# Kernel optimization log

Hardware: AMD Instinct MI355X
Metric: run time of the kernel (lower is better)

Reference implementation:

```python
import jax, jax.numpy as jnp
import numpy as np


def _maxpool(x, k):
    # non-overlapping kxk max pool (kernel == stride), NCHW
    B, C, H, W = x.shape
    return x.reshape(B, C, H // k, k, W // k, k).max(axis=(3, 5))


def setup_inputs() -> dict:
    key = jax.random.key(0)
    k1, k2, k3, k4 = jax.random.split(key, 4)
    return {
        "x1": jax.random.normal(k1, (8, 128, 128, 128), dtype=jnp.float32),
        "x2": jax.random.normal(k2, (8, 32, 256, 256), dtype=jnp.float32),
        "x3": jax.random.normal(k3, (8, 2, 512, 512), dtype=jnp.float32),
        "pure_ff": jax.random.normal(k4, (8, 256, 64, 64), dtype=jnp.float32),
    }


def reference(x1, x2, x3, pure_ff):
    # torch.cat([x,x],1) repeated n times duplicates the whole channel block
    # 2^n times; pooling duplicated channels equals pooling once then tiling.
    y1 = jnp.tile(_maxpool(x1, 2), (1, 2, 1, 1))    # 1 cat  -> x2 channels
    y2 = jnp.tile(_maxpool(x2, 4), (1, 8, 1, 1))    # 3 cats -> x8 channels
    y3 = jnp.tile(_maxpool(x3, 8), (1, 128, 1, 1))  # 7 cats -> x128 channels
    return jax.nn.relu(y1 + y2 + y3 + pure_ff)
```

## Files before the change

kernel.cpp:

```cpp
#include <hip/hip_runtime.h>
#include <math.h>


__global__ __launch_bounds__(256, 8) void fused_ff_block3(
    const float* __restrict__ x1, const float* __restrict__ x2,
    const float* __restrict__ x3, const float* __restrict__ ff,
    float* __restrict__ out)
{
    __shared__ float y2s[32][16];
    __shared__ float y3s[2][16];

    const int bid = blockIdx.x;
    const int wq  = bid & 3;
    const int h   = (bid >> 2) & 63;
    const int b   = bid >> 8;
    const int tid = threadIdx.x;

    const int lane = tid & 63;
    const int o3   = (tid >> 6) * 8 + (lane >> 3);
    const int r3   = lane & 7;
    const int c3   = o3 >> 4;
    const int w3   = o3 & 15;
    const float* p3 = x3 + (size_t)b * 524288 + (size_t)c3 * 262144
                    + (size_t)(h * 8 + r3) * 512 + (size_t)(wq * 16 + w3) * 8;
    const float4 a3 = *reinterpret_cast<const float4*>(p3);
    const float4 b3 = *reinterpret_cast<const float4*>(p3 + 4);

    #pragma unroll
    for (int it = 0; it < 2; ++it) {
        const int v  = tid + it * 256;
        const int c2 = v >> 4;
        const int w2 = v & 15;
        const float* p = x2 + (size_t)b * 2097152 + (size_t)c2 * 65536
                       + (size_t)(h * 4) * 256 + (size_t)(wq * 16 + w2) * 4;
        const float4 q0 = *reinterpret_cast<const float4*>(p);
        const float4 q1 = *reinterpret_cast<const float4*>(p + 256);
        const float4 q2 = *reinterpret_cast<const float4*>(p + 512);
        const float4 q3 = *reinterpret_cast<const float4*>(p + 768);
        float m = fmaxf(fmaxf(fmaxf(q0.x, q0.y), fmaxf(q0.z, q0.w)),
                        fmaxf(fmaxf(q1.x, q1.y), fmaxf(q1.z, q1.w)));
        m = fmaxf(m, fmaxf(fmaxf(q2.x, q2.y), fmaxf(q2.z, q2.w)));
        m = fmaxf(m, fmaxf(fmaxf(q3.x, q3.y), fmaxf(q3.z, q3.w)));
        y2s[c2][w2] = m;
    }

    float m3 = fmaxf(fmaxf(fmaxf(a3.x, a3.y), fmaxf(a3.z, a3.w)),
                     fmaxf(fmaxf(b3.x, b3.y), fmaxf(b3.z, b3.w)));
    m3 = fmaxf(m3, __shfl_xor(m3, 1, 64));
    m3 = fmaxf(m3, __shfl_xor(m3, 2, 64));
    m3 = fmaxf(m3, __shfl_xor(m3, 4, 64));
    if (r3 == 0) y3s[c3][w3] = m3;

    __syncthreads();

    const int w4  = tid & 3;
    const int c1b = tid >> 2;
    #pragma unroll
    for (int it = 0; it < 2; ++it) {
        const int c1 = c1b + it * 64;
        const float* p = x1 + (size_t)b * 2097152 + (size_t)c1 * 16384
                       + (size_t)(h * 2) * 128 + (size_t)(wq * 16 + w4 * 4) * 2;
        const float4 a0 = *reinterpret_cast<const float4*>(p);
        const float4 a1 = *reinterpret_cast<const float4*>(p + 4);
        const float4 r0 = *reinterpret_cast<const float4*>(p + 128);
        const float4 r1 = *reinterpret_cast<const float4*>(p + 132);
        float4 y1v;
        y1v.x = fmaxf(fmaxf(a0.x, a0.y), fmaxf(r0.x, r0.y));
        y1v.y = fmaxf(fmaxf(a0.z, a0.w), fmaxf(r0.z, r0.w));
        y1v.z = fmaxf(fmaxf(a1.x, a1.y), fmaxf(r1.x, r1.y));
        y1v.w = fmaxf(fmaxf(a1.z, a1.w), fmaxf(r1.z, r1.w));

        const float4 y2v = *reinterpret_cast<const float4*>(&y2s[c1 & 31][w4 * 4]);
        const float4 y3v = *reinterpret_cast<const float4*>(&y3s[c1 & 1][w4 * 4]);

        const size_t o0 = (size_t)b * 1048576 + (size_t)c1 * 4096
                        + (size_t)h * 64 + (size_t)(wq * 16 + w4 * 4);
        const size_t o1 = o0 + (size_t)128 * 4096;
        const float4 f0 = *reinterpret_cast<const float4*>(ff + o0);
        const float4 f1 = *reinterpret_cast<const float4*>(ff + o1);

        float4 s;
        s.x = y1v.x + y2v.x + y3v.x;
        s.y = y1v.y + y2v.y + y3v.y;
        s.z = y1v.z + y2v.z + y3v.z;
        s.w = y1v.w + y2v.w + y3v.w;

        float4 u0, u1;
        u0.x = fmaxf(s.x + f0.x, 0.0f);
        u0.y = fmaxf(s.y + f0.y, 0.0f);
        u0.z = fmaxf(s.z + f0.z, 0.0f);
        u0.w = fmaxf(s.w + f0.w, 0.0f);
        u1.x = fmaxf(s.x + f1.x, 0.0f);
        u1.y = fmaxf(s.y + f1.y, 0.0f);
        u1.z = fmaxf(s.z + f1.z, 0.0f);
        u1.w = fmaxf(s.w + f1.w, 0.0f);

        *reinterpret_cast<float4*>(out + o0) = u0;
        *reinterpret_cast<float4*>(out + o1) = u1;
    }
}

extern "C" void kernel_launch(void* const* d_in, const int* in_sizes, int n_in,
                              void* d_out, int out_size, void* d_ws, size_t ws_size,
                              hipStream_t stream) {
    const float* x1 = (const float*)d_in[0];
    const float* x2 = (const float*)d_in[1];
    const float* x3 = (const float*)d_in[2];
    const float* ff = (const float*)d_in[3];
    float* out = (float*)d_out;

    dim3 grid(2048);
    dim3 block(256);
    fused_ff_block3<<<grid, block, 0, stream>>>(x1, x2, x3, ff, out);
}
```

Baseline: 41.57 us.

## Process full output row per block with 1024-thread blocks

Each block now covers all 64 output columns of one row (instead of a 16-wide quarter), using 1024 threads and 512 blocks. This makes each row access to x1, x2, x3 and ff a longer contiguous span and removes the per-quarter index math. It reduces the grid to 512 blocks on a 256-CU device, so there are only about two large blocks per CU, which can leave less room to hide memory latency. The shared arrays are padded to 68 columns.

```diff
diff --git a/kernel.cpp b/kernel.cpp
--- a/kernel.cpp
+++ b/kernel.cpp
@@ -2,37 +2,43 @@
 #include <math.h>
 
 
-__global__ __launch_bounds__(256, 8) void fused_ff_block3(
+__global__ __launch_bounds__(1024, 8) void fused_ff_block3(
     const float* __restrict__ x1, const float* __restrict__ x2,
     const float* __restrict__ x3, const float* __restrict__ ff,
     float* __restrict__ out)
 {
-    __shared__ float y2s[32][16];
-    __shared__ float y3s[2][16];
+    __shared__ float y2s[32][68];
+    __shared__ float y3s[2][68];
 
     const int bid = blockIdx.x;
-    const int wq  = bid & 3;
-    const int h   = (bid >> 2) & 63;
-    const int b   = bid >> 8;
+    const int b   = bid >> 6;
+    const int h   = bid & 63;
     const int tid = threadIdx.x;
 
-    const int lane = tid & 63;
-    const int o3   = (tid >> 6) * 8 + (lane >> 3);
-    const int r3   = lane & 7;
-    const int c3   = o3 >> 4;
-    const int w3   = o3 & 15;
-    const float* p3 = x3 + (size_t)b * 524288 + (size_t)c3 * 262144
-                    + (size_t)(h * 8 + r3) * 512 + (size_t)(wq * 16 + w3) * 8;
-    const float4 a3 = *reinterpret_cast<const float4*>(p3);
-    const float4 b3 = *reinterpret_cast<const float4*>(p3 + 4);
+    {
+        const int o3 = tid >> 3;
+        const int r3 = tid & 7;
+        const int c3 = o3 >> 6;
+        const int w3 = o3 & 63;
+        const float* p = x3 + (size_t)b * 524288 + (size_t)c3 * 262144
+                       + (size_t)(h * 8 + r3) * 512 + (size_t)w3 * 8;
+        const float4 a = *reinterpret_cast<const float4*>(p);
+        const float4 c = *reinterpret_cast<const float4*>(p + 4);
+        float m = fmaxf(fmaxf(fmaxf(a.x, a.y), fmaxf(a.z, a.w)),
+                        fmaxf(fmaxf(c.x, c.y), fmaxf(c.z, c.w)));
+        m = fmaxf(m, __shfl_xor(m, 1, 64));
+        m = fmaxf(m, __shfl_xor(m, 2, 64));
+        m = fmaxf(m, __shfl_xor(m, 4, 64));
+        if (r3 == 0) y3s[c3][w3] = m;
+    }
 
     #pragma unroll
     for (int it = 0; it < 2; ++it) {
-        const int v  = tid + it * 256;
-        const int c2 = v >> 4;
-        const int w2 = v & 15;
+        const int v  = tid + it * 1024;
+        const int c2 = v >> 6;
+        const int w2 = v & 63;
         const float* p = x2 + (size_t)b * 2097152 + (size_t)c2 * 65536
-                       + (size_t)(h * 4) * 256 + (size_t)(wq * 16 + w2) * 4;
+                       + (size_t)(h * 4) * 256 + (size_t)w2 * 4;
         const float4 q0 = *reinterpret_cast<const float4*>(p);
         const float4 q1 = *reinterpret_cast<const float4*>(p + 256);
         const float4 q2 = *reinterpret_cast<const float4*>(p + 512);
@@ -44,22 +50,15 @@
         y2s[c2][w2] = m;
     }
 
-    float m3 = fmaxf(fmaxf(fmaxf(a3.x, a3.y), fmaxf(a3.z, a3.w)),
-                     fmaxf(fmaxf(b3.x, b3.y), fmaxf(b3.z, b3.w)));
-    m3 = fmaxf(m3, __shfl_xor(m3, 1, 64));
-    m3 = fmaxf(m3, __shfl_xor(m3, 2, 64));
-    m3 = fmaxf(m3, __shfl_xor(m3, 4, 64));
-    if (r3 == 0) y3s[c3][w3] = m3;
-
     __syncthreads();
 
-    const int w4  = tid & 3;
-    const int c1b = tid >> 2;
+    const int w4  = tid & 15;
+    const int c10 = tid >> 4;
     #pragma unroll
     for (int it = 0; it < 2; ++it) {
-        const int c1 = c1b + it * 64;
+        const int c1 = c10 + it * 64;
         const float* p = x1 + (size_t)b * 2097152 + (size_t)c1 * 16384
-                       + (size_t)(h * 2) * 128 + (size_t)(wq * 16 + w4 * 4) * 2;
+                       + (size_t)(h * 2) * 128 + (size_t)w4 * 8;
         const float4 a0 = *reinterpret_cast<const float4*>(p);
         const float4 a1 = *reinterpret_cast<const float4*>(p + 4);
         const float4 r0 = *reinterpret_cast<const float4*>(p + 128);
@@ -74,7 +73,7 @@
         const float4 y3v = *reinterpret_cast<const float4*>(&y3s[c1 & 1][w4 * 4]);
 
         const size_t o0 = (size_t)b * 1048576 + (size_t)c1 * 4096
-                        + (size_t)h * 64 + (size_t)(wq * 16 + w4 * 4);
+                        + (size_t)h * 64 + (size_t)w4 * 4;
         const size_t o1 = o0 + (size_t)128 * 4096;
         const float4 f0 = *reinterpret_cast<const float4*>(ff + o0);
         const float4 f1 = *reinterpret_cast<const float4*>(ff + o1);
@@ -109,7 +108,7 @@
     const float* ff = (const float*)d_in[3];
     float* out = (float*)d_out;
 
-    dim3 grid(2048);
-    dim3 block(256);
+    dim3 grid(512);
+    dim3 block(1024);
     fused_ff_block3<<<grid, block, 0, stream>>>(x1, x2, x3, ff, out);
 }
```

Measured after the change: 40.36 us. 2.9% less time.
